# Kernel tuning notes

Measured on AMD Instinct MI355X. Metric: run time of the kernel, lower is better.

The kernel has to match this reference:

```python
import jax
jax.config.update("jax_enable_x64", True)
import jax.numpy as jnp
import numpy as np

CKA_WEIGHT = 0.1


def _group_cka_sum(feats):
    """feats: [F, N, D] float. Returns sum of pairwise CKA over all (i,j) pairs.

    Faithful to CKASR: K = X X^T with zeroed diagonal, unbiased HSIC
    (Song et al. estimator), CKA[i,j] = HSIC(Ki,Kj)/sqrt(HSIC(Ki,Ki)HSIC(Kj,Kj)).
    All pairwise loops are batched into einsums.
    """
    F, N, D = feats.shape
    X = feats.reshape(F, N, D).astype(jnp.float64)
    K = jnp.einsum('fnd,fmd->fnm', X, X)                 # [F,N,N] Gram
    K = K * (1.0 - jnp.eye(N, dtype=K.dtype))            # fill_diagonal_(0)
    # HSIC(Ki, Kj) = 1/(N(N-3)) * ( tr(Ki Kj)
    #   + sum(Ki) sum(Kj) / ((N-1)(N-2))
    #   - 2/(N-2) * <rowsum(Ki), rowsum(Kj)> )
    trKL = jnp.einsum('iab,jab->ij', K, K)               # tr(Ki Kj), K symmetric
    s = jnp.sum(K, axis=(1, 2))                          # [F] total sums
    r = jnp.sum(K, axis=2)                               # [F,N] row sums
    rr = jnp.einsum('ia,ja->ij', r, r)                   # [F,F]
    hsic = (trKL + jnp.outer(s, s) / ((N - 1) * (N - 2))
            - 2.0 * rr / (N - 2)) / (N * (N - 3))        # [F,F]
    d = jnp.sqrt(jnp.diagonal(hsic))                     # [F]
    cka = hsic / (d[:, None] * d[None, :])
    return jnp.sum(cka)


def setup_inputs() -> dict:
    key = jax.random.key(0)
    k1, k2, k3, k4 = jax.random.split(key, 4)
    N, C = 64, 1000
    output = jax.random.normal(k1, (N, C), dtype=jnp.float32)
    target = jax.random.randint(k2, (N,), 0, C, dtype=jnp.int64)
    feats_a = jax.random.normal(k3, (3, N, 65536), dtype=jnp.float32)
    feats_b = jax.random.normal(k4, (4, N, 32768), dtype=jnp.float32)
    return {"output": output, "target": target,
            "feats_a": feats_a, "feats_b": feats_b}


def reference(output, target, feats_a, feats_b):
    N = output.shape[0]
    logp = jax.nn.log_softmax(output.astype(jnp.float32), axis=-1)
    ce = -jnp.mean(logp[jnp.arange(N), target])           # CrossEntropyLoss (mean)
    cka = _group_cka_sum(feats_a) + _group_cka_sum(feats_b)
    loss = ce + CKA_WEIGHT * cka.astype(jnp.float32)
    return (loss, output)
```

## Files before the change

### kernel.cpp

```cpp
#include <hip/hip_runtime.h>
#include <hip/hip_bf16.h>
#include <math.h>

typedef __attribute__((ext_vector_type(8))) short short8;
typedef __attribute__((ext_vector_type(4))) float f32x4;

#define PSTRIDE 4160
#define SLAB_A_F 8388608u
#define SLAB_B_F 4194304u

__device__ __forceinline__ unsigned int bf16_rn(float x) {
    unsigned int u = __float_as_uint(x);
    return (u + 0x7FFFu + ((u >> 16) & 1u)) >> 16;
}

__global__ __launch_bounds__(256) void ce_kernel(
    const float* __restrict__ logits, const int* __restrict__ target,
    float* __restrict__ out_copy, float* __restrict__ ce_rows)
{
    const int row = blockIdx.x;
    const float* x = logits + row * 1000;
    const int t = threadIdx.x;
    __shared__ float red[256];

    float m = -INFINITY;
    for (int i = t; i < 1000; i += 256) {
        float v = x[i];
        out_copy[row * 1000 + i] = v;
        m = fmaxf(m, v);
    }
    red[t] = m; __syncthreads();
    for (int s = 128; s > 0; s >>= 1) {
        if (t < s) red[t] = fmaxf(red[t], red[t + s]);
        __syncthreads();
    }
    m = red[0];
    __syncthreads();

    float ssum = 0.f;
    for (int i = t; i < 1000; i += 256) ssum += expf(x[i] - m);
    red[t] = ssum; __syncthreads();
    for (int s = 128; s > 0; s >>= 1) {
        if (t < s) red[t] += red[t + s];
        __syncthreads();
    }
    if (t == 0) {
        double lse = (double)m + log((double)red[0]);
        int tg = target[row];
        ce_rows[row] = (float)(-((double)x[tg] - lse));
    }
}

__global__ __launch_bounds__(256) void repack_kernel(
    const float* __restrict__ A, const float* __restrict__ B,
    char* __restrict__ slab, int nfA, int nfB)
{
    const int uA = nfA * 512;
    const int uTot = uA + nfB * 256;
    const int t = threadIdx.x;

    for (int u = blockIdx.x; u < uTot; u += gridDim.x) {
        const float* xr;
        char* slabF;
        int row, seg, D;
        if (u < uA) {
            int f = u >> 9, rem = u & 511;
            seg = rem & 7; row = rem >> 3; D = 65536;
            xr = A + ((size_t)(f * 64 + row)) * D;
            slabF = slab + (size_t)f * SLAB_A_F;
        } else {
            int v = u - uA;
            int f = v >> 8, rem = v & 255;
            seg = rem & 3; row = rem >> 2; D = 32768;
            xr = B + ((size_t)(f * 64 + row)) * D;
            slabF = slab + (size_t)nfA * SLAB_A_F + (size_t)f * SLAB_B_F;
        }
        const int k0 = seg * 8192;
        float4 va[4], vb[4];
#pragma unroll
        for (int i = 0; i < 4; ++i) {
            const float* p = xr + k0 + i * 2048 + t * 8;
            va[i] = *(const float4*)p;
            vb[i] = *(const float4*)(p + 4);
        }
#pragma unroll
        for (int i = 0; i < 4; ++i) {
            float vv[8] = {va[i].x, va[i].y, va[i].z, va[i].w,
                           vb[i].x, vb[i].y, vb[i].z, vb[i].w};
            short8 hv;
#pragma unroll
            for (int j = 0; j < 8; ++j) hv[j] = (short)bf16_rn(vv[j]);
            int kg = k0 + i * 2048 + t * 8;
            int chunk = kg >> 9, kk = kg & 511;
            *(short8*)(slabF + (size_t)chunk * 65536 + row * 1024 + kk * 2) = hv;
        }
    }
}

__global__ __launch_bounds__(256) void gram_kernel(
    const char* __restrict__ slab, float* __restrict__ partials,
    int nfA, int nfB)
{
    __shared__ float kbuf[4096];
    const int blk = blockIdx.x;
    const int f = blk >> 6, local = blk & 63;

    const char* slabF;
    int c0, nchunk;
    if (f < nfA) {
        slabF = slab + (size_t)f * SLAB_A_F;
        c0 = local * 2; nchunk = 2;
    } else {
        slabF = slab + (size_t)nfA * SLAB_A_F + (size_t)(f - nfA) * SLAB_B_F;
        c0 = local; nchunk = 1;
    }

    const int t = threadIdx.x;
    const int wave = t >> 6, lane = t & 63;
    const int m = lane & 15, quad = lane >> 4;
    const int loff = wave * 256 + quad * 16;

    f32x4 acc[4][4];
#pragma unroll
    for (int i = 0; i < 4; ++i)
#pragma unroll
        for (int j = 0; j < 4; ++j) acc[i][j] = (f32x4)0.f;

    for (int ci = 0; ci < nchunk; ++ci) {
        const char* cb = slabF + (size_t)(c0 + ci) * 65536;
        short8 fr[4][4];
#pragma unroll
        for (int s = 0; s < 4; ++s)
#pragma unroll
            for (int tm = 0; tm < 4; ++tm)
                fr[s][tm] = *(const short8*)(cb + (tm * 16 + m) * 1024
                                             + loff + s * 64);
#pragma unroll
        for (int s = 0; s < 4; ++s)
#pragma unroll
            for (int tm = 0; tm < 4; ++tm)
#pragma unroll
                for (int tn = 0; tn < 4; ++tn)
                    acc[tm][tn] = __builtin_amdgcn_mfma_f32_16x16x32_bf16(
                        fr[s][tm], fr[s][tn], acc[tm][tn], 0, 0, 0);
    }

    __syncthreads();
    if (wave == 0) {
#pragma unroll
        for (int tm = 0; tm < 4; ++tm)
#pragma unroll
            for (int tn = 0; tn < 4; ++tn)
#pragma unroll
                for (int r = 0; r < 4; ++r)
                    kbuf[(tm * 16 + quad * 4 + r) * 64 + tn * 16 + m] = acc[tm][tn][r];
    }
    __syncthreads();
    if (wave != 0) {
#pragma unroll
        for (int tm = 0; tm < 4; ++tm)
#pragma unroll
            for (int tn = 0; tn < 4; ++tn)
#pragma unroll
                for (int r = 0; r < 4; ++r)
                    atomicAdd(&kbuf[(tm * 16 + quad * 4 + r) * 64 + tn * 16 + m],
                              acc[tm][tn][r]);
    }
    __syncthreads();

    float4* outp = (float4*)(partials + (size_t)blk * PSTRIDE);
    const float4* kb4 = (const float4*)kbuf;
    for (int e = t; e < 1024; e += 256) outp[e] = kb4[e];
}

__global__ __launch_bounds__(256) void reduce_kernel(
    const float* __restrict__ partials, float* __restrict__ K, int singleF)
{
    __shared__ double red[256];
    int f, eblk, base;
    if (singleF < 0) { f = blockIdx.x >> 6; eblk = blockIdx.x & 63; base = f * 64; }
    else             { f = singleF; eblk = blockIdx.x; base = 0; }
    const int e = (eblk << 6) + (threadIdx.x & 63);
    const int jg = threadIdx.x >> 6;

    double s0 = 0.0, s1 = 0.0;
    for (int j = jg; j < 64; j += 8) {
        s0 += (double)partials[(size_t)(base + j) * PSTRIDE + e];
        s1 += (double)partials[(size_t)(base + j + 4) * PSTRIDE + e];
    }
    red[threadIdx.x] = s0 + s1;
    __syncthreads();
    if (jg == 0) {
        double tot = red[threadIdx.x] + red[threadIdx.x + 64]
                   + red[threadIdx.x + 128] + red[threadIdx.x + 192];
        int rr = e >> 6, cc = e & 63;
        K[f * 4096 + e] = (rr == cc) ? 0.f : (float)tot;
    }
}

__global__ __launch_bounds__(256) void hsic_kernel(
    const float* __restrict__ K, double* __restrict__ hsic_out)
{
    const int p = blockIdx.x;
    int i, j;
    if (p < 9) { i = p / 3; j = p % 3; }
    else       { int q = p - 9; i = 3 + q / 4; j = 3 + q % 4; }
    const float* Ki = K + i * 4096;
    const float* Kj = K + j * 4096;
    const int t = threadIdx.x;

    __shared__ double red[256];
    __shared__ double ri[64], rj[64];

    double local = 0.0;
    for (int e = t; e < 4096; e += 256)
        local += (double)Ki[e] * (double)Kj[e];
    red[t] = local; __syncthreads();
    for (int s = 128; s > 0; s >>= 1) {
        if (t < s) red[t] += red[t + s];
        __syncthreads();
    }

    if (t < 64) {
        double s = 0.0;
        for (int mc = 0; mc < 64; ++mc) s += (double)Ki[t * 64 + mc];
        ri[t] = s;
    } else if (t < 128) {
        int n = t - 64;
        double s = 0.0;
        for (int mc = 0; mc < 64; ++mc) s += (double)Kj[n * 64 + mc];
        rj[n] = s;
    }
    __syncthreads();

    if (t == 0) {
        double tr = red[0];
        double rr = 0.0, si = 0.0, sj = 0.0;
        for (int n = 0; n < 64; ++n) {
            rr += ri[n] * rj[n];
            si += ri[n];
            sj += rj[n];
        }
        const double N = 64.0;
        const double c1 = (N - 1.0) * (N - 2.0);
        const double c2 = N - 2.0;
        const double c3 = N * (N - 3.0);
        hsic_out[p] = (tr + si * sj / c1 - 2.0 * rr / c2) / c3;
    }
}

__global__ __launch_bounds__(64) void final_kernel(
    const double* __restrict__ hsic, const float* __restrict__ ce_rows,
    float* __restrict__ out_loss)
{
    if (threadIdx.x != 0) return;
    double ce = 0.0;
    for (int n = 0; n < 64; ++n) ce += (double)ce_rows[n];
    ce /= 64.0;

    double cka_total = 0.0;
    for (int i = 0; i < 3; ++i)
        for (int j = 0; j < 3; ++j)
            cka_total += hsic[i * 3 + j] / sqrt(hsic[i * 3 + i] * hsic[j * 3 + j]);
    for (int i = 0; i < 4; ++i)
        for (int j = 0; j < 4; ++j)
            cka_total += hsic[9 + i * 4 + j] / sqrt(hsic[9 + i * 4 + i] * hsic[9 + j * 4 + j]);

    out_loss[0] = (float)(ce + 0.1 * cka_total);
}

extern "C" void kernel_launch(void* const* d_in, const int* in_sizes, int n_in,
                              void* d_out, int out_size, void* d_ws, size_t ws_size,
                              hipStream_t stream)
{
    const float* output  = (const float*)d_in[0];
    const int*   target  = (const int*)d_in[1];
    const float* feats_a = (const float*)d_in[2];
    const float* feats_b = (const float*)d_in[3];
    float* out = (float*)d_out;

    char* ws = (char*)d_ws;
    float*  K       = (float*)ws;
    float*  ce_rows = (float*)(ws + 114688);
    double* hsic    = (double*)(ws + 114944);
    char*   slab    = ws + 131072;

    const size_t slabAll = 3 * (size_t)SLAB_A_F + 4 * (size_t)SLAB_B_F;
    const size_t partMain = (size_t)448 * PSTRIDE * 4;
    const size_t mainNeed = 131072 + slabAll + partMain;

    hipLaunchKernelGGL(ce_kernel, dim3(64), dim3(256), 0, stream,
                       output, target, out + 1, ce_rows);

    if (ws_size >= mainNeed) {
        float* partials = (float*)(slab + slabAll);
        hipLaunchKernelGGL(repack_kernel, dim3(1280), dim3(256), 0, stream,
                           feats_a, feats_b, slab, 3, 4);
        hipLaunchKernelGGL(gram_kernel, dim3(448), dim3(256), 0, stream,
                           (const char*)slab, partials, 3, 4);
        hipLaunchKernelGGL(reduce_kernel, dim3(448), dim3(256), 0, stream,
                           partials, K, -1);
    } else {
        float* partials = (float*)(slab + SLAB_A_F);
        for (int f = 0; f < 7; ++f) {
            if (f < 3) {
                const float* X = feats_a + (size_t)f * 64 * 65536;
                hipLaunchKernelGGL(repack_kernel, dim3(256), dim3(256), 0, stream,
                                   X, (const float*)nullptr, slab, 1, 0);
                hipLaunchKernelGGL(gram_kernel, dim3(64), dim3(256), 0, stream,
                                   (const char*)slab, partials, 1, 0);
            } else {
                const float* X = feats_b + (size_t)(f - 3) * 64 * 32768;
                hipLaunchKernelGGL(repack_kernel, dim3(128), dim3(256), 0, stream,
                                   (const float*)nullptr, X, slab, 0, 1);
                hipLaunchKernelGGL(gram_kernel, dim3(64), dim3(256), 0, stream,
                                   (const char*)slab, partials, 0, 1);
            }
            hipLaunchKernelGGL(reduce_kernel, dim3(64), dim3(256), 0, stream,
                               partials, K, f);
        }
    }

    hipLaunchKernelGGL(hsic_kernel, dim3(25), dim3(256), 0, stream, K, hsic);
    hipLaunchKernelGGL(final_kernel, dim3(1), dim3(64), 0, stream,
                       hsic, ce_rows, out);
}
```

Before: 179.7 us.

## Fuse bf16 repack into Gram kernel via swizzled LDS staging

Drops the separate repack pass that converted fp32 features to bf16 and wrote them to a global slab. Each Gram block now loads its 512-column chunk straight from the fp32 input, converts to bf16 into XOR-swizzled shared memory, and runs the MFMA Gram product from LDS. This removes a full global write and re-read of the bf16 copy plus one kernel launch. The cost is more blocks, 640 partial Gram outputs instead of 448, and a reduce step that sums 128 partials for the larger features.

```diff
diff --git a/kernel.cpp b/kernel.cpp
--- a/kernel.cpp
+++ b/kernel.cpp
@@ -6,8 +6,6 @@
 typedef __attribute__((ext_vector_type(4))) float f32x4;
 
 #define PSTRIDE 4160
-#define SLAB_A_F 8388608u
-#define SLAB_B_F 4194304u
 
 __device__ __forceinline__ unsigned int bf16_rn(float x) {
     unsigned int u = __float_as_uint(x);
@@ -51,72 +49,45 @@
     }
 }
 
-__global__ __launch_bounds__(256) void repack_kernel(
+__global__ __launch_bounds__(256) void gramf_kernel(
     const float* __restrict__ A, const float* __restrict__ B,
-    char* __restrict__ slab, int nfA, int nfB)
-{
-    const int uA = nfA * 512;
-    const int uTot = uA + nfB * 256;
-    const int t = threadIdx.x;
-
-    for (int u = blockIdx.x; u < uTot; u += gridDim.x) {
-        const float* xr;
-        char* slabF;
-        int row, seg, D;
-        if (u < uA) {
-            int f = u >> 9, rem = u & 511;
-            seg = rem & 7; row = rem >> 3; D = 65536;
-            xr = A + ((size_t)(f * 64 + row)) * D;
-            slabF = slab + (size_t)f * SLAB_A_F;
-        } else {
-            int v = u - uA;
-            int f = v >> 8, rem = v & 255;
-            seg = rem & 3; row = rem >> 2; D = 32768;
-            xr = B + ((size_t)(f * 64 + row)) * D;
-            slabF = slab + (size_t)nfA * SLAB_A_F + (size_t)f * SLAB_B_F;
-        }
-        const int k0 = seg * 8192;
-        float4 va[4], vb[4];
-#pragma unroll
-        for (int i = 0; i < 4; ++i) {
-            const float* p = xr + k0 + i * 2048 + t * 8;
-            va[i] = *(const float4*)p;
-            vb[i] = *(const float4*)(p + 4);
-        }
-#pragma unroll
-        for (int i = 0; i < 4; ++i) {
-            float vv[8] = {va[i].x, va[i].y, va[i].z, va[i].w,
-                           vb[i].x, vb[i].y, vb[i].z, vb[i].w};
-            short8 hv;
-#pragma unroll
-            for (int j = 0; j < 8; ++j) hv[j] = (short)bf16_rn(vv[j]);
-            int kg = k0 + i * 2048 + t * 8;
-            int chunk = kg >> 9, kk = kg & 511;
-            *(short8*)(slabF + (size_t)chunk * 65536 + row * 1024 + kk * 2) = hv;
-        }
-    }
-}
-
-__global__ __launch_bounds__(256) void gram_kernel(
-    const char* __restrict__ slab, float* __restrict__ partials,
-    int nfA, int nfB)
-{
-    __shared__ float kbuf[4096];
+    float* __restrict__ partials, int nfA, int nfB)
+{
+    __shared__ f32x4 ldsv[4096];
+    char* lds = (char*)ldsv;
+
     const int blk = blockIdx.x;
-    const int f = blk >> 6, local = blk & 63;
-
-    const char* slabF;
-    int c0, nchunk;
-    if (f < nfA) {
-        slabF = slab + (size_t)f * SLAB_A_F;
-        c0 = local * 2; nchunk = 2;
+    const int uA = nfA * 128;
+    const float* xf;
+    int c, D;
+    if (blk < uA) {
+        int f = blk >> 7; c = blk & 127; D = 65536;
+        xf = A + (size_t)f * 64 * 65536;
     } else {
-        slabF = slab + (size_t)nfA * SLAB_A_F + (size_t)(f - nfA) * SLAB_B_F;
-        c0 = local; nchunk = 1;
+        int v = blk - uA;
+        int f = v >> 6; c = v & 63; D = 32768;
+        xf = B + (size_t)f * 64 * 32768;
     }
 
     const int t = threadIdx.x;
     const int wave = t >> 6, lane = t & 63;
+    const int k0 = c * 512;
+
+#pragma unroll 4
+    for (int rr = 0; rr < 16; ++rr) {
+        const int row = wave * 16 + rr;
+        const float* p = xf + (size_t)row * D + k0 + lane * 8;
+        float4 va = *(const float4*)p;
+        float4 vb = *(const float4*)(p + 4);
+        float vv[8] = {va.x, va.y, va.z, va.w, vb.x, vb.y, vb.z, vb.w};
+        short8 hv;
+#pragma unroll
+        for (int j = 0; j < 8; ++j) hv[j] = (short)bf16_rn(vv[j]);
+        const int boff = (lane * 16) ^ ((row & 7) << 4);
+        *(short8*)(lds + row * 1024 + boff) = hv;
+    }
+    __syncthreads();
+
     const int m = lane & 15, quad = lane >> 4;
     const int loff = wave * 256 + quad * 16;
 
@@ -126,26 +97,26 @@
 #pragma unroll
         for (int j = 0; j < 4; ++j) acc[i][j] = (f32x4)0.f;
 
-    for (int ci = 0; ci < nchunk; ++ci) {
-        const char* cb = slabF + (size_t)(c0 + ci) * 65536;
-        short8 fr[4][4];
-#pragma unroll
-        for (int s = 0; s < 4; ++s)
-#pragma unroll
-            for (int tm = 0; tm < 4; ++tm)
-                fr[s][tm] = *(const short8*)(cb + (tm * 16 + m) * 1024
-                                             + loff + s * 64);
-#pragma unroll
-        for (int s = 0; s < 4; ++s)
-#pragma unroll
-            for (int tm = 0; tm < 4; ++tm)
-#pragma unroll
-                for (int tn = 0; tn < 4; ++tn)
-                    acc[tm][tn] = __builtin_amdgcn_mfma_f32_16x16x32_bf16(
-                        fr[s][tm], fr[s][tn], acc[tm][tn], 0, 0, 0);
-    }
-
-    __syncthreads();
+    short8 fr[4][4];
+#pragma unroll
+    for (int s = 0; s < 4; ++s)
+#pragma unroll
+        for (int tm = 0; tm < 4; ++tm) {
+            const int row = tm * 16 + m;
+            const int boff = (loff + s * 64) ^ ((row & 7) << 4);
+            fr[s][tm] = *(const short8*)(lds + row * 1024 + boff);
+        }
+#pragma unroll
+    for (int s = 0; s < 4; ++s)
+#pragma unroll
+        for (int tm = 0; tm < 4; ++tm)
+#pragma unroll
+            for (int tn = 0; tn < 4; ++tn)
+                acc[tm][tn] = __builtin_amdgcn_mfma_f32_16x16x32_bf16(
+                    fr[s][tm], fr[s][tn], acc[tm][tn], 0, 0, 0);
+
+    __syncthreads();
+    float* kbuf = (float*)lds;
     if (wave == 0) {
 #pragma unroll
         for (int tm = 0; tm < 4; ++tm)
@@ -177,14 +148,20 @@
     const float* __restrict__ partials, float* __restrict__ K, int singleF)
 {
     __shared__ double red[256];
-    int f, eblk, base;
-    if (singleF < 0) { f = blockIdx.x >> 6; eblk = blockIdx.x & 63; base = f * 64; }
-    else             { f = singleF; eblk = blockIdx.x; base = 0; }
+    int f, eblk, base, count;
+    if (singleF < 0) {
+        f = blockIdx.x >> 6; eblk = blockIdx.x & 63;
+        if (f < 3) { base = f * 128;            count = 128; }
+        else       { base = 384 + (f - 3) * 64; count = 64;  }
+    } else {
+        f = singleF; eblk = blockIdx.x; base = 0;
+        count = (f < 3) ? 128 : 64;
+    }
     const int e = (eblk << 6) + (threadIdx.x & 63);
     const int jg = threadIdx.x >> 6;
 
     double s0 = 0.0, s1 = 0.0;
-    for (int j = jg; j < 64; j += 8) {
+    for (int j = jg; j < count; j += 8) {
         s0 += (double)partials[(size_t)(base + j) * PSTRIDE + e];
         s1 += (double)partials[(size_t)(base + j + 4) * PSTRIDE + e];
     }
@@ -283,38 +260,29 @@
     float*  K       = (float*)ws;
     float*  ce_rows = (float*)(ws + 114688);
     double* hsic    = (double*)(ws + 114944);
-    char*   slab    = ws + 131072;
-
-    const size_t slabAll = 3 * (size_t)SLAB_A_F + 4 * (size_t)SLAB_B_F;
-    const size_t partMain = (size_t)448 * PSTRIDE * 4;
-    const size_t mainNeed = 131072 + slabAll + partMain;
+    float*  partials = (float*)(ws + 131072);
+
+    const size_t partMain = (size_t)640 * PSTRIDE * 4;
+    const size_t mainNeed = 131072 + partMain;
 
     hipLaunchKernelGGL(ce_kernel, dim3(64), dim3(256), 0, stream,
                        output, target, out + 1, ce_rows);
 
     if (ws_size >= mainNeed) {
-        float* partials = (float*)(slab + slabAll);
-        hipLaunchKernelGGL(repack_kernel, dim3(1280), dim3(256), 0, stream,
-                           feats_a, feats_b, slab, 3, 4);
-        hipLaunchKernelGGL(gram_kernel, dim3(448), dim3(256), 0, stream,
-                           (const char*)slab, partials, 3, 4);
+        hipLaunchKernelGGL(gramf_kernel, dim3(640), dim3(256), 0, stream,
+                           feats_a, feats_b, partials, 3, 4);
         hipLaunchKernelGGL(reduce_kernel, dim3(448), dim3(256), 0, stream,
                            partials, K, -1);
     } else {
-        float* partials = (float*)(slab + SLAB_A_F);
         for (int f = 0; f < 7; ++f) {
             if (f < 3) {
                 const float* X = feats_a + (size_t)f * 64 * 65536;
-                hipLaunchKernelGGL(repack_kernel, dim3(256), dim3(256), 0, stream,
-                                   X, (const float*)nullptr, slab, 1, 0);
-                hipLaunchKernelGGL(gram_kernel, dim3(64), dim3(256), 0, stream,
-                                   (const char*)slab, partials, 1, 0);
+                hipLaunchKernelGGL(gramf_kernel, dim3(128), dim3(256), 0, stream,
+                                   X, (const float*)nullptr, partials, 1, 0);
             } else {
                 const float* X = feats_b + (size_t)(f - 3) * 64 * 32768;
-                hipLaunchKernelGGL(repack_kernel, dim3(128), dim3(256), 0, stream,
-                                   (const float*)nullptr, X, slab, 0, 1);
-                hipLaunchKernelGGL(gram_kernel, dim3(64), dim3(256), 0, stream,
-                                   (const char*)slab, partials, 0, 1);
+                hipLaunchKernelGGL(gramf_kernel, dim3(64), dim3(256), 0, stream,
+                                   (const float*)nullptr, X, partials, 0, 1);
             }
             hipLaunchKernelGGL(reduce_kernel, dim3(64), dim3(256), 0, stream,
                                partials, K, f);
```

Measured after the change: 182.1 us. No clear change (+1.3%).
